# Kernel tuning notes

Measured on AMD Instinct MI355X. Metric: run time of the kernel, lower is better.

Reference implementation:

```python
import jax, jax.numpy as jnp
import numpy as np

N_NODES = 50000
N_EDGES = 1600000
D = 64  # d_hidden // n_groups = 128 // 2
EPS = 1e-5


def setup_inputs() -> dict:
    key = jax.random.key(0)
    ks = jax.random.split(key, 6)
    x = jax.random.normal(ks[0], (N_NODES, D), dtype=jnp.float32)
    edge_index = jax.random.randint(ks[1], (2, N_EDGES), 0, N_NODES)
    dropout_mask = jax.random.uniform(ks[2], (N_NODES, D), dtype=jnp.float32)
    # LayerNorm affine params (elementwise_affine=True)
    gamma = jnp.ones((D,), jnp.float32)
    beta = jnp.zeros((D,), jnp.float32)
    # SAGEConv params: lin_l (applied to mean-aggregated neighbors, has bias),
    # lin_r (applied to root features, no bias) -- PyG defaults.
    lim = 1.0 / np.sqrt(D)
    W_l = jax.random.uniform(ks[3], (D, D), jnp.float32, -lim, lim)
    b_l = jnp.zeros((D,), jnp.float32)
    W_r = jax.random.uniform(ks[4], (D, D), jnp.float32, -lim, lim)
    return {"x": x, "dropout_mask": dropout_mask, "gamma": gamma, "beta": beta,
            "W_l": W_l, "b_l": b_l, "W_r": W_r, "edge_index": edge_index}


def reference(x, dropout_mask, gamma, beta, W_l, b_l, W_r, edge_index):
    # LayerNorm over feature dim, then ReLU, then dropout-mask multiply
    mu = jnp.mean(x, axis=-1, keepdims=True)
    var = jnp.mean((x - mu) ** 2, axis=-1, keepdims=True)
    h = (x - mu) * jax.lax.rsqrt(var + EPS) * gamma + beta  # [N, D]
    h = jax.nn.relu(h) * dropout_mask
    # SAGEConv (mean aggregation): gather source features, segment-mean by dst
    src, dst = edge_index[0], edge_index[1]
    msg = h[src]  # [E, D] edge-indexed gather
    agg = jax.ops.segment_sum(msg, dst, num_segments=N_NODES)  # [N, D]
    cnt = jax.ops.segment_sum(jnp.ones((msg.shape[0],), h.dtype), dst,
                              num_segments=N_NODES)
    agg = agg / jnp.maximum(cnt, 1.0)[:, None]  # scatter_mean (0 for isolated nodes)
    # out = lin_l(agg) + lin_r(h)
    return agg @ W_l.T + b_l + h @ W_r.T
```

## Files before the change

kernel.cpp:

```cpp
#include <hip/hip_runtime.h>

#define N_NODES 50000
#define N_EDGES 1600000
#define D 64
#define CAP 96
#define CHUNK 4096
#define NCHUNK ((N_EDGES + CHUNK - 1) / CHUNK)
#define NBUCK 196

typedef _Float16 f16x2 __attribute__((ext_vector_type(2)));

static __device__ __forceinline__ float dot2acc(f16x2 a, f16x2 b, float c) {
#if __has_builtin(__builtin_amdgcn_fdot2)
  return __builtin_amdgcn_fdot2(a, b, c, false);
#else
  return c + (float)a.x * (float)b.x + (float)a.y * (float)b.y;
#endif
}

static __device__ __forceinline__ f16x2 shflx2(f16x2 v, int msk) {
  return __builtin_bit_cast(
      f16x2, (unsigned)__shfl_xor((int)__builtin_bit_cast(unsigned, v), msk, 64));
}

static __device__ __forceinline__ void gpair(
    int myA, int myB, int off, int o, const char* hb, int coff,
    f16x2* aA, f16x2* aB) {
  uint4 va[4], vb[4];
#pragma unroll
  for (int j = 0; j < 4; ++j) {
    int ia = __shfl(myA, off + j * 8 + o, 64);
    va[j] = *(const uint4*)(hb + ((ia << 7) | coff));
  }
#pragma unroll
  for (int j = 0; j < 4; ++j) {
    int ib = __shfl(myB, off + j * 8 + o, 64);
    vb[j] = *(const uint4*)(hb + ((ib << 7) | coff));
  }
#pragma unroll
  for (int j = 0; j < 4; ++j) {
    aA[0] += __builtin_bit_cast(f16x2, va[j].x);
    aA[1] += __builtin_bit_cast(f16x2, va[j].y);
    aA[2] += __builtin_bit_cast(f16x2, va[j].z);
    aA[3] += __builtin_bit_cast(f16x2, va[j].w);
    aB[0] += __builtin_bit_cast(f16x2, vb[j].x);
    aB[1] += __builtin_bit_cast(f16x2, vb[j].y);
    aB[2] += __builtin_bit_cast(f16x2, vb[j].z);
    aB[3] += __builtin_bit_cast(f16x2, vb[j].w);
  }
}

__global__ __launch_bounds__(256) void k_ln(
    const float* __restrict__ x, const float* __restrict__ mask,
    const float* __restrict__ gamma, const float* __restrict__ beta,
    f16x2* __restrict__ hf2) {
  int tid = blockIdx.x * blockDim.x + threadIdx.x;
  int n = tid >> 6;
  int d = tid & 63;
  if (n > N_NODES) return;
  if (n == N_NODES) {
    if ((d & 1) == 0) {
      f16x2 z;
      z.x = (_Float16)0.f;
      z.y = (_Float16)0.f;
      hf2[(size_t)n * 32 + (d >> 1)] = z;
    }
    return;
  }
  float v = x[n * D + d];
  float s = v, s2 = v * v;
#pragma unroll
  for (int off = 32; off >= 1; off >>= 1) {
    s += __shfl_xor(s, off, 64);
    s2 += __shfl_xor(s2, off, 64);
  }
  float mu = s * (1.0f / D);
  float var = fmaxf(s2 * (1.0f / D) - mu * mu, 0.0f);
  float hv = (v - mu) * rsqrtf(var + 1e-5f) * gamma[d] + beta[d];
  hv = fmaxf(hv, 0.0f) * mask[n * D + d];
  float hn = __shfl_xor(hv, 1, 64);
  if ((d & 1) == 0) {
    f16x2 p;
    p.x = (_Float16)hv;
    p.y = (_Float16)hn;
    hf2[(size_t)n * 32 + (d >> 1)] = p;
  }
}

__global__ __launch_bounds__(256) void k_hist(
    const int* __restrict__ ei, int* __restrict__ ghistT) {
  __shared__ int lhist[NBUCK];
  int b = blockIdx.x;
  int base = b * CHUNK;
  int len = min(CHUNK, N_EDGES - base);
  for (int i = threadIdx.x; i < NBUCK; i += 256) lhist[i] = 0;
  __syncthreads();
  const int4* pd = (const int4*)(ei + N_EDGES + base);
  for (int i = threadIdx.x; i < (len >> 2); i += 256) {
    int4 v = pd[i];
    atomicAdd(&lhist[((unsigned)v.x) >> 8], 1);
    atomicAdd(&lhist[((unsigned)v.y) >> 8], 1);
    atomicAdd(&lhist[((unsigned)v.z) >> 8], 1);
    atomicAdd(&lhist[((unsigned)v.w) >> 8], 1);
  }
  __syncthreads();
  for (int k = threadIdx.x; k < NBUCK; k += 256) ghistT[k * NCHUNK + b] = lhist[k];
}

__global__ __launch_bounds__(256) void k_scan1(
    const int* __restrict__ ghistT, int* __restrict__ chunkbaseT,
    int* __restrict__ total) {
  __shared__ int sbuf[2][512];
  int k = blockIdx.x;
  int t = threadIdx.x;
  int v0 = (t < NCHUNK) ? ghistT[k * NCHUNK + t] : 0;
  int v1 = (t + 256 < NCHUNK) ? ghistT[k * NCHUNK + t + 256] : 0;
  sbuf[0][t] = v0;
  sbuf[0][t + 256] = v1;
  __syncthreads();
  int cur = 0;
#pragma unroll
  for (int off = 1; off < 512; off <<= 1) {
    int a0 = sbuf[cur][t] + ((t >= off) ? sbuf[cur][t - off] : 0);
    int a1 = sbuf[cur][t + 256] + ((t + 256 >= off) ? sbuf[cur][t + 256 - off] : 0);
    sbuf[cur ^ 1][t] = a0;
    sbuf[cur ^ 1][t + 256] = a1;
    __syncthreads();
    cur ^= 1;
  }
  if (t < NCHUNK) chunkbaseT[k * NCHUNK + t] = sbuf[cur][t] - v0;
  if (t + 256 < NCHUNK) chunkbaseT[k * NCHUNK + t + 256] = sbuf[cur][t + 256] - v1;
  if (t == 0) total[k] = sbuf[cur][NCHUNK - 1];
}

__global__ __launch_bounds__(256) void k_scan2(
    const int* __restrict__ total, int* __restrict__ bucket_start,
    const float* __restrict__ Wl, const float* __restrict__ Wr,
    f16x2* __restrict__ wf16) {
  if (blockIdx.x > 0) {
    int g = (blockIdx.x - 1) * 256 + threadIdx.x;
    float2 v = (g < 2048) ? ((const float2*)Wl)[g] : ((const float2*)Wr)[g - 2048];
    f16x2 p;
    p.x = (_Float16)v.x;
    p.y = (_Float16)v.y;
    wf16[g] = p;
    return;
  }
  __shared__ int sbuf[2][256];
  int t = threadIdx.x;
  int v = (t < NBUCK) ? total[t] : 0;
  sbuf[0][t] = v;
  __syncthreads();
  int cur = 0;
#pragma unroll
  for (int off = 1; off < 256; off <<= 1) {
    int a = sbuf[cur][t] + ((t >= off) ? sbuf[cur][t - off] : 0);
    sbuf[cur ^ 1][t] = a;
    __syncthreads();
    cur ^= 1;
  }
  if (t < NBUCK) bucket_start[t] = sbuf[cur][t] - v;
  if (t == 0) bucket_start[NBUCK] = N_EDGES;
}

__global__ __launch_bounds__(256) void k_scatter2(
    const int* __restrict__ ei, const int* __restrict__ chunkbaseT,
    const int* __restrict__ bucket_start, unsigned* __restrict__ sorted) {
  __shared__ int lcur[NBUCK];
  int b = blockIdx.x;
  int base = b * CHUNK;
  int len = min(CHUNK, N_EDGES - base);
  for (int k = threadIdx.x; k < NBUCK; k += 256)
    lcur[k] = bucket_start[k] + chunkbaseT[k * NCHUNK + b];
  __syncthreads();
  const int4* ps = (const int4*)(ei + base);
  const int4* pd = (const int4*)(ei + N_EDGES + base);
  for (int i = threadIdx.x; i < (len >> 2); i += 256) {
    int4 s4 = ps[i];
    int4 d4 = pd[i];
    {
      unsigned dst = (unsigned)d4.x, src = (unsigned)s4.x;
      int pos = atomicAdd(&lcur[dst >> 8], 1);
      sorted[pos] = (dst << 16) | src;
    }
    {
      unsigned dst = (unsigned)d4.y, src = (unsigned)s4.y;
      int pos = atomicAdd(&lcur[dst >> 8], 1);
      sorted[pos] = (dst << 16) | src;
    }
    {
      unsigned dst = (unsigned)d4.z, src = (unsigned)s4.z;
      int pos = atomicAdd(&lcur[dst >> 8], 1);
      sorted[pos] = (dst << 16) | src;
    }
    {
      unsigned dst = (unsigned)d4.w, src = (unsigned)s4.w;
      int pos = atomicAdd(&lcur[dst >> 8], 1);
      sorted[pos] = (dst << 16) | src;
    }
  }
}

__global__ __launch_bounds__(1024) void k_place3(
    const unsigned* __restrict__ sorted, const int* __restrict__ bucket_start,
    unsigned short* __restrict__ adj, int* __restrict__ cnt) {
  __shared__ int lcnt[256];
  int k = blockIdx.x;
  if (threadIdx.x < 256) lcnt[threadIdx.x] = 0;
  __syncthreads();
  int s = bucket_start[k];
  int e = bucket_start[k + 1];
  for (int i = s + threadIdx.x; i < e; i += 1024) {
    unsigned rec = sorted[i];
    int dst = (int)(rec >> 16);
    int pos = atomicAdd(&lcnt[dst & 255], 1);
    if (pos < CAP) adj[(size_t)dst * CAP + pos] = (unsigned short)(rec & 0xffffu);
  }
  __syncthreads();
  if (threadIdx.x < 256) {
    int dst = (k << 8) + threadIdx.x;
    if (dst < N_NODES) {
      int c0 = lcnt[threadIdx.x];
      cnt[dst] = c0;
      int p0 = min(c0, CAP);
      int p1 = min((p0 + 7) & ~7, CAP);
      for (int i = p0; i < p1; ++i)
        adj[(size_t)dst * CAP + i] = (unsigned short)N_NODES;
    }
  }
}

__global__ __launch_bounds__(512, 6) void k_gather_out(
    const f16x2* __restrict__ hf2, const int* __restrict__ cnt,
    const unsigned short* __restrict__ adj, const f16x2* __restrict__ wf16,
    const float* __restrict__ bl, float* __restrict__ out) {
  __shared__ f16x2 sWl2[D][34];
  __shared__ f16x2 sWr2[D][34];
  __shared__ f16x2 sA2[16][32];
  __shared__ f16x2 sH2[16][32];
  int w = threadIdx.x >> 6;
  int L = threadIdx.x & 63;
  {
    int i0 = threadIdx.x * 4;
    int row = i0 >> 5, col = i0 & 31;
    const f16x2* wl = wf16;
    const f16x2* wr = wf16 + 2048;
#pragma unroll
    for (int j = 0; j < 4; ++j) {
      sWl2[row][col + j] = wl[i0 + j];
      sWr2[row][col + j] = wr[i0 + j];
    }
  }
  __syncthreads();

  int nA = blockIdx.x * 16 + w * 2;
  int nB = nA + 1;
  int degA = min(__builtin_nontemporal_load(cnt + nA), CAP);
  int degB = min(__builtin_nontemporal_load(cnt + nB), CAP);
  int degpA = min((degA + 7) & ~7, CAP);
  int degpB = min((degB + 7) & ~7, CAP);
  int mx = max(degpA, degpB);
  int o = L >> 3;
  int c8 = L & 7;
  int coff = c8 << 4;
  const char* hb = (const char*)hf2;
  int abA = nA * CAP, abB = nB * CAP;

  int mA = min(degpA, 64), mB = min(degpB, 64);
  int myA = (L < mA) ? (int)__builtin_nontemporal_load(adj + abA + L) : N_NODES;
  int myB = (L < mB) ? (int)__builtin_nontemporal_load(adj + abB + L) : N_NODES;

  f16x2 aA[4], aB[4];
#pragma unroll
  for (int t = 0; t < 4; ++t) {
    aA[t] = __builtin_bit_cast(f16x2, 0u);
    aB[t] = __builtin_bit_cast(f16x2, 0u);
  }
  gpair(myA, myB, 0, o, hb, coff, aA, aB);
  if (mx > 32) gpair(myA, myB, 32, o, hb, coff, aA, aB);
  if (mx > 64) {
    int mA2 = max(degpA - 64, 0), mB2 = max(degpB - 64, 0);
    int myA2 = (L < mA2) ? (int)__builtin_nontemporal_load(adj + abA + 64 + L)
                         : N_NODES;
    int myB2 = (L < mB2) ? (int)__builtin_nontemporal_load(adj + abB + 64 + L)
                         : N_NODES;
    gpair(myA2, myB2, 0, o, hb, coff, aA, aB);
  }

#pragma unroll
  for (int msk = 8; msk <= 32; msk <<= 1) {
#pragma unroll
    for (int t = 0; t < 4; ++t) {
      aA[t] += shflx2(aA[t], msk);
      aB[t] += shflx2(aB[t], msk);
    }
  }
  float invA = 1.0f / (float)max(degA, 1);
  float invB = 1.0f / (float)max(degB, 1);
  if (o == 0) {
#pragma unroll
    for (int t = 0; t < 4; ++t) {
      f16x2 p;
      p.x = (_Float16)((float)aA[t].x * invA);
      p.y = (_Float16)((float)aA[t].y * invA);
      sA2[2 * w][4 * c8 + t] = p;
    }
  } else if (o == 1) {
#pragma unroll
    for (int t = 0; t < 4; ++t) {
      f16x2 p;
      p.x = (_Float16)((float)aB[t].x * invB);
      p.y = (_Float16)((float)aB[t].y * invB);
      sA2[2 * w + 1][4 * c8 + t] = p;
    }
  }
  if (L < 32) sH2[2 * w][L] = hf2[(size_t)nA * 32 + L];
  else sH2[2 * w + 1][L - 32] = hf2[(size_t)nB * 32 + (L - 32)];

  float accA = bl[L];
  float accB = accA;
#pragma unroll
  for (int k2 = 0; k2 < 32; ++k2) {
    f16x2 wlv = sWl2[L][k2];
    f16x2 wrv = sWr2[L][k2];
    accA = dot2acc(sA2[2 * w][k2], wlv, accA);
    accA = dot2acc(sH2[2 * w][k2], wrv, accA);
    accB = dot2acc(sA2[2 * w + 1][k2], wlv, accB);
    accB = dot2acc(sH2[2 * w + 1][k2], wrv, accB);
  }
  __builtin_nontemporal_store(accA, out + (size_t)nA * D + L);
  __builtin_nontemporal_store(accB, out + (size_t)nB * D + L);
}

extern "C" void kernel_launch(void* const* d_in, const int* in_sizes, int n_in,
                              void* d_out, int out_size, void* d_ws,
                              size_t ws_size, hipStream_t stream) {
  const float* x = (const float*)d_in[0];
  const float* mask = (const float*)d_in[1];
  const float* gamma = (const float*)d_in[2];
  const float* beta = (const float*)d_in[3];
  const float* Wl = (const float*)d_in[4];
  const float* bl = (const float*)d_in[5];
  const float* Wr = (const float*)d_in[6];
  const int* ei = (const int*)d_in[7];
  float* out = (float*)d_out;

  f16x2* hf2 = (f16x2*)d_ws;
  unsigned* sorted = (unsigned*)(hf2 + (size_t)(N_NODES + 1) * 32);
  int* ghistT = (int*)(sorted + (size_t)N_EDGES);
  int* chunkbaseT = ghistT + NBUCK * NCHUNK;
  int* total = chunkbaseT + NBUCK * NCHUNK;
  int* bucket_start = total + NBUCK;
  int* cnt = bucket_start + (NBUCK + 2);
  unsigned short* adj = (unsigned short*)(cnt + N_NODES);
  f16x2* wf16 = (f16x2*)(adj + (size_t)N_NODES * CAP);

  dim3 blk(256);
  int g1 = ((N_NODES + 1) * D + 255) / 256;
  k_ln<<<g1, blk, 0, stream>>>(x, mask, gamma, beta, hf2);
  k_hist<<<NCHUNK, blk, 0, stream>>>(ei, ghistT);
  k_scan1<<<NBUCK, blk, 0, stream>>>(ghistT, chunkbaseT, total);
  k_scan2<<<17, blk, 0, stream>>>(total, bucket_start, Wl, Wr, wf16);
  k_scatter2<<<NCHUNK, blk, 0, stream>>>(ei, chunkbaseT, bucket_start, sorted);
  k_place3<<<NBUCK, dim3(1024), 0, stream>>>(sorted, bucket_start, adj, cnt);
  k_gather_out<<<N_NODES / 16, dim3(512), 0, stream>>>(hf2, cnt, adj, wf16, bl, out);
}
```

Before: 78.67 us.

## Fuse layernorm, histogram and adjacency prefill into one front kernel; ballot-driven gather

```diff
diff --git a/kernel.cpp b/kernel.cpp
--- a/kernel.cpp
+++ b/kernel.cpp
@@ -7,6 +7,13 @@
 #define CHUNK 4096
 #define NCHUNK ((N_EDGES + CHUNK - 1) / CHUNK)
 #define NBUCK 196
+#define DUMMY 0xFFFF
+#define NROWS 65536
+#define G_LNB 12500
+#define G_HIST0 (G_LNB + 1)
+#define G_FILL0 (G_HIST0 + NCHUNK)
+#define ADJ_U4 (N_NODES * CAP * 2 / 16)
+#define FILLB ((ADJ_U4 + 1023) / 1024)
 
 typedef _Float16 f16x2 __attribute__((ext_vector_type(2)));
 
@@ -50,23 +57,54 @@
   }
 }
 
-__global__ __launch_bounds__(256) void k_ln(
+__global__ __launch_bounds__(256) void k_front(
     const float* __restrict__ x, const float* __restrict__ mask,
     const float* __restrict__ gamma, const float* __restrict__ beta,
-    f16x2* __restrict__ hf2) {
-  int tid = blockIdx.x * blockDim.x + threadIdx.x;
-  int n = tid >> 6;
-  int d = tid & 63;
-  if (n > N_NODES) return;
-  if (n == N_NODES) {
-    if ((d & 1) == 0) {
+    f16x2* __restrict__ hf2, const int* __restrict__ ei,
+    int* __restrict__ ghistT, uint4* __restrict__ adj4) {
+  __shared__ int lhist[NBUCK];
+  int b = blockIdx.x;
+  if (b >= G_FILL0) {
+    int base = (b - G_FILL0) * 1024;
+    uint4 f;
+    f.x = f.y = f.z = f.w = 0xFFFFFFFFu;
+#pragma unroll
+    for (int j = 0; j < 4; ++j) {
+      int i = base + j * 256 + threadIdx.x;
+      if (i < ADJ_U4) adj4[i] = f;
+    }
+    return;
+  }
+  if (b >= G_HIST0) {
+    int base = (b - G_HIST0) * CHUNK;
+    int len = min(CHUNK, N_EDGES - base);
+    for (int i = threadIdx.x; i < NBUCK; i += 256) lhist[i] = 0;
+    __syncthreads();
+    const int4* pd = (const int4*)(ei + N_EDGES + base);
+    for (int i = threadIdx.x; i < (len >> 2); i += 256) {
+      int4 v = pd[i];
+      atomicAdd(&lhist[((unsigned)v.x) >> 8], 1);
+      atomicAdd(&lhist[((unsigned)v.y) >> 8], 1);
+      atomicAdd(&lhist[((unsigned)v.z) >> 8], 1);
+      atomicAdd(&lhist[((unsigned)v.w) >> 8], 1);
+    }
+    __syncthreads();
+    for (int k = threadIdx.x; k < NBUCK; k += 256)
+      ghistT[k * NCHUNK + (b - G_HIST0)] = lhist[k];
+    return;
+  }
+  if (b == G_LNB) {
+    if (threadIdx.x < 32) {
       f16x2 z;
       z.x = (_Float16)0.f;
       z.y = (_Float16)0.f;
-      hf2[(size_t)n * 32 + (d >> 1)] = z;
+      hf2[(size_t)DUMMY * 32 + threadIdx.x] = z;
     }
     return;
   }
+  int tid = b * 256 + threadIdx.x;
+  int n = tid >> 6;
+  int d = tid & 63;
   float v = x[n * D + d];
   float s = v, s2 = v * v;
 #pragma unroll
@@ -85,26 +123,6 @@
     p.y = (_Float16)hn;
     hf2[(size_t)n * 32 + (d >> 1)] = p;
   }
-}
-
-__global__ __launch_bounds__(256) void k_hist(
-    const int* __restrict__ ei, int* __restrict__ ghistT) {
-  __shared__ int lhist[NBUCK];
-  int b = blockIdx.x;
-  int base = b * CHUNK;
-  int len = min(CHUNK, N_EDGES - base);
-  for (int i = threadIdx.x; i < NBUCK; i += 256) lhist[i] = 0;
-  __syncthreads();
-  const int4* pd = (const int4*)(ei + N_EDGES + base);
-  for (int i = threadIdx.x; i < (len >> 2); i += 256) {
-    int4 v = pd[i];
-    atomicAdd(&lhist[((unsigned)v.x) >> 8], 1);
-    atomicAdd(&lhist[((unsigned)v.y) >> 8], 1);
-    atomicAdd(&lhist[((unsigned)v.z) >> 8], 1);
-    atomicAdd(&lhist[((unsigned)v.w) >> 8], 1);
-  }
-  __syncthreads();
-  for (int k = threadIdx.x; k < NBUCK; k += 256) ghistT[k * NCHUNK + b] = lhist[k];
 }
 
 __global__ __launch_bounds__(256) void k_scan1(
@@ -163,19 +181,19 @@
   if (t == 0) bucket_start[NBUCK] = N_EDGES;
 }
 
-__global__ __launch_bounds__(256) void k_scatter2(
+__global__ __launch_bounds__(512) void k_scatter2(
     const int* __restrict__ ei, const int* __restrict__ chunkbaseT,
     const int* __restrict__ bucket_start, unsigned* __restrict__ sorted) {
   __shared__ int lcur[NBUCK];
   int b = blockIdx.x;
   int base = b * CHUNK;
   int len = min(CHUNK, N_EDGES - base);
-  for (int k = threadIdx.x; k < NBUCK; k += 256)
+  for (int k = threadIdx.x; k < NBUCK; k += 512)
     lcur[k] = bucket_start[k] + chunkbaseT[k * NCHUNK + b];
   __syncthreads();
   const int4* ps = (const int4*)(ei + base);
   const int4* pd = (const int4*)(ei + N_EDGES + base);
-  for (int i = threadIdx.x; i < (len >> 2); i += 256) {
+  for (int i = threadIdx.x; i < (len >> 2); i += 512) {
     int4 s4 = ps[i];
     int4 d4 = pd[i];
     {
@@ -203,7 +221,7 @@
 
 __global__ __launch_bounds__(1024) void k_place3(
     const unsigned* __restrict__ sorted, const int* __restrict__ bucket_start,
-    unsigned short* __restrict__ adj, int* __restrict__ cnt) {
+    unsigned short* __restrict__ adj, float* __restrict__ invd) {
   __shared__ int lcnt[256];
   int k = blockIdx.x;
   if (threadIdx.x < 256) lcnt[threadIdx.x] = 0;
@@ -219,19 +237,13 @@
   __syncthreads();
   if (threadIdx.x < 256) {
     int dst = (k << 8) + threadIdx.x;
-    if (dst < N_NODES) {
-      int c0 = lcnt[threadIdx.x];
-      cnt[dst] = c0;
-      int p0 = min(c0, CAP);
-      int p1 = min((p0 + 7) & ~7, CAP);
-      for (int i = p0; i < p1; ++i)
-        adj[(size_t)dst * CAP + i] = (unsigned short)N_NODES;
-    }
+    if (dst < N_NODES)
+      invd[dst] = 1.0f / (float)max(min(lcnt[threadIdx.x], CAP), 1);
   }
 }
 
 __global__ __launch_bounds__(512, 6) void k_gather_out(
-    const f16x2* __restrict__ hf2, const int* __restrict__ cnt,
+    const f16x2* __restrict__ hf2, const float* __restrict__ invd,
     const unsigned short* __restrict__ adj, const f16x2* __restrict__ wf16,
     const float* __restrict__ bl, float* __restrict__ out) {
   __shared__ f16x2 sWl2[D][34];
@@ -255,20 +267,19 @@
 
   int nA = blockIdx.x * 16 + w * 2;
   int nB = nA + 1;
-  int degA = min(__builtin_nontemporal_load(cnt + nA), CAP);
-  int degB = min(__builtin_nontemporal_load(cnt + nB), CAP);
-  int degpA = min((degA + 7) & ~7, CAP);
-  int degpB = min((degB + 7) & ~7, CAP);
-  int mx = max(degpA, degpB);
+  int abA = nA * CAP, abB = nB * CAP;
+  int myA = (int)__builtin_nontemporal_load(adj + abA + L);
+  int myB = (int)__builtin_nontemporal_load(adj + abB + L);
+  float invA = __builtin_nontemporal_load(invd + nA);
+  float invB = __builtin_nontemporal_load(invd + nB);
+
+  unsigned long long bm =
+      __ballot(myA != DUMMY) | __ballot(myB != DUMMY);
+
   int o = L >> 3;
   int c8 = L & 7;
   int coff = c8 << 4;
   const char* hb = (const char*)hf2;
-  int abA = nA * CAP, abB = nB * CAP;
-
-  int mA = min(degpA, 64), mB = min(degpB, 64);
-  int myA = (L < mA) ? (int)__builtin_nontemporal_load(adj + abA + L) : N_NODES;
-  int myB = (L < mB) ? (int)__builtin_nontemporal_load(adj + abB + L) : N_NODES;
 
   f16x2 aA[4], aB[4];
 #pragma unroll
@@ -277,13 +288,12 @@
     aB[t] = __builtin_bit_cast(f16x2, 0u);
   }
   gpair(myA, myB, 0, o, hb, coff, aA, aB);
-  if (mx > 32) gpair(myA, myB, 32, o, hb, coff, aA, aB);
-  if (mx > 64) {
-    int mA2 = max(degpA - 64, 0), mB2 = max(degpB - 64, 0);
-    int myA2 = (L < mA2) ? (int)__builtin_nontemporal_load(adj + abA + 64 + L)
-                         : N_NODES;
-    int myB2 = (L < mB2) ? (int)__builtin_nontemporal_load(adj + abB + 64 + L)
-                         : N_NODES;
+  if ((bm >> 32) != 0ull) gpair(myA, myB, 32, o, hb, coff, aA, aB);
+  if ((bm >> 63) != 0ull) {
+    int myA2 = (L < 32) ? (int)__builtin_nontemporal_load(adj + abA + 64 + L)
+                        : DUMMY;
+    int myB2 = (L < 32) ? (int)__builtin_nontemporal_load(adj + abB + 64 + L)
+                        : DUMMY;
     gpair(myA2, myB2, 0, o, hb, coff, aA, aB);
   }
 
@@ -295,8 +305,6 @@
       aB[t] += shflx2(aB[t], msk);
     }
   }
-  float invA = 1.0f / (float)max(degA, 1);
-  float invB = 1.0f / (float)max(degB, 1);
   if (o == 0) {
 #pragma unroll
     for (int t = 0; t < 4; ++t) {
@@ -346,22 +354,23 @@
   float* out = (float*)d_out;
 
   f16x2* hf2 = (f16x2*)d_ws;
-  unsigned* sorted = (unsigned*)(hf2 + (size_t)(N_NODES + 1) * 32);
+  unsigned* sorted = (unsigned*)(hf2 + (size_t)NROWS * 32);
   int* ghistT = (int*)(sorted + (size_t)N_EDGES);
   int* chunkbaseT = ghistT + NBUCK * NCHUNK;
   int* total = chunkbaseT + NBUCK * NCHUNK;
   int* bucket_start = total + NBUCK;
-  int* cnt = bucket_start + (NBUCK + 2);
-  unsigned short* adj = (unsigned short*)(cnt + N_NODES);
+  float* invd = (float*)(bucket_start + (NBUCK + 2));
+  unsigned short* adj = (unsigned short*)(invd + N_NODES);
   f16x2* wf16 = (f16x2*)(adj + (size_t)N_NODES * CAP);
 
   dim3 blk(256);
-  int g1 = ((N_NODES + 1) * D + 255) / 256;
-  k_ln<<<g1, blk, 0, stream>>>(x, mask, gamma, beta, hf2);
-  k_hist<<<NCHUNK, blk, 0, stream>>>(ei, ghistT);
+  k_front<<<G_FILL0 + FILLB, blk, 0, stream>>>(x, mask, gamma, beta, hf2, ei,
+                                               ghistT, (uint4*)adj);
   k_scan1<<<NBUCK, blk, 0, stream>>>(ghistT, chunkbaseT, total);
   k_scan2<<<17, blk, 0, stream>>>(total, bucket_start, Wl, Wr, wf16);
-  k_scatter2<<<NCHUNK, blk, 0, stream>>>(ei, chunkbaseT, bucket_start, sorted);
-  k_place3<<<NBUCK, dim3(1024), 0, stream>>>(sorted, bucket_start, adj, cnt);
-  k_gather_out<<<N_NODES / 16, dim3(512), 0, stream>>>(hf2, cnt, adj, wf16, bl, out);
-}
+  k_scatter2<<<NCHUNK, dim3(512), 0, stream>>>(ei, chunkbaseT, bucket_start,
+                                               sorted);
+  k_place3<<<NBUCK, dim3(1024), 0, stream>>>(sorted, bucket_start, adj, invd);
+  k_gather_out<<<N_NODES / 16, dim3(512), 0, stream>>>(hf2, invd, adj, wf16,
+                                                       bl, out);
+}
```

Result: faster. 75.09 us, median of 3 (-4.5%).
